# Kernel optimization log

Measured on AMD Instinct MI355X. Metric: run time of the kernel, lower is better.

## Reference

```python
import jax, jax.numpy as jnp
import numpy as np

B, C, H, W = 4, 8, 64, 64
C8 = C // 8  # = 1, required for the residual broadcast in PAM


def _conv1x1(x, w, b):
    # x: [B,C,H,W], w: [O,C], b: [O] -> [B,O,H,W]
    return jnp.einsum('bchw,oc->bohw', x, w) + b[None, :, None, None]


def setup_inputs() -> dict:
    key = jax.random.key(0)
    ks = jax.random.split(key, 13)
    s_c = 1.0 / np.sqrt(C)
    inp = {'x': jax.random.normal(ks[0], (B, C, H, W), jnp.float32)}
    # CAM: three 1x1 convs C->C
    inp['cam_wq'] = jax.random.normal(ks[1], (C, C), jnp.float32) * s_c
    inp['cam_bq'] = jnp.zeros((C,), jnp.float32)
    inp['cam_wk'] = jax.random.normal(ks[2], (C, C), jnp.float32) * s_c
    inp['cam_bk'] = jnp.zeros((C,), jnp.float32)
    inp['cam_wv'] = jax.random.normal(ks[3], (C, C), jnp.float32) * s_c
    inp['cam_bv'] = jnp.zeros((C,), jnp.float32)
    # PAM: three 1x1 convs C->C//8
    inp['pam_wq'] = jax.random.normal(ks[4], (C8, C), jnp.float32) * s_c
    inp['pam_bq'] = jnp.zeros((C8,), jnp.float32)
    inp['pam_wk'] = jax.random.normal(ks[5], (C8, C), jnp.float32) * s_c
    inp['pam_bk'] = jnp.zeros((C8,), jnp.float32)
    inp['pam_wv'] = jax.random.normal(ks[6], (C8, C), jnp.float32) * s_c
    inp['pam_bv'] = jnp.zeros((C8,), jnp.float32)
    return inp


def reference(x, cam_wq, cam_bq, cam_wk, cam_bk, cam_wv, cam_bv,
              pam_wq, pam_bq, pam_wk, pam_bk, pam_wv, pam_bv):
    b, c, h, w = x.shape
    hw = h * w

    # ---- Channel Attention Module (C x C attention) ----
    q = _conv1x1(x, cam_wq, cam_bq).reshape(b, c, hw)            # [B,C,HW]
    k = _conv1x1(x, cam_wk, cam_bk).reshape(b, c, hw)            # [B,C,HW]
    v = _conv1x1(x, cam_wv, cam_bv).reshape(b, c, hw)            # [B,C,HW]
    attn_c = jax.nn.softmax(jnp.einsum('bcn,bdn->bcd', q, k), axis=-1)  # [B,C,C]
    out_cam = jnp.einsum('bcd,bdn->bcn', attn_c, v).reshape(b, c, h, w) + x

    # ---- Pixel Attention Module (HW x HW attention, C//8 channels) ----
    pq = _conv1x1(x, pam_wq, pam_bq).reshape(b, -1, hw)          # [B,C8,HW]
    pk = _conv1x1(x, pam_wk, pam_bk).reshape(b, -1, hw)          # [B,C8,HW]
    pv = _conv1x1(x, pam_wv, pam_bv).reshape(b, -1, hw)          # [B,C8,HW]
    attn_p = jax.nn.softmax(jnp.einsum('bcn,bcm->bnm', pq, pk), axis=-1)  # [B,HW,HW]
    # out = v @ attn^T  -> [B,C8,HW]; residual broadcasts C8=1 against C
    out_p = jnp.einsum('bcm,bnm->bcn', pv, attn_p).reshape(b, c // 8, h, w)
    out_pam = out_p + x                                          # broadcast [B,1,H,W]+[B,C,H,W]

    return out_pam + out_cam
```

## Files before the change

### kernel.cpp

```cpp
#include <hip/hip_runtime.h>

#define CC 8
#define HW 4096
#define L2E 1.4426950408889634f

typedef __attribute__((ext_vector_type(4))) float f32x4;

__global__ __launch_bounds__(64) void kGram(const float* __restrict__ x,
                                            float* __restrict__ ws)
{
  const int b = blockIdx.x >> 6, chunk = blockIdx.x & 63;
  const int ln = threadIdx.x;
  const int n = chunk * 64 + ln;
  const float* xb = x + b * CC * HW;

  float xv[CC];
  #pragma unroll
  for (int c = 0; c < CC; ++c) xv[c] = xb[c * HW + n];

  float acc[44];
  {
    int k = 0;
    #pragma unroll
    for (int c = 0; c < CC; ++c) {
      #pragma unroll
      for (int d = c; d < CC; ++d) { acc[k] = xv[c] * xv[d]; ++k; }
    }
    #pragma unroll
    for (int c = 0; c < CC; ++c) acc[36 + c] = xv[c];
  }
  #pragma unroll
  for (int i = 0; i < 44; ++i) {
    float v = acc[i];
    #pragma unroll
    for (int off = 32; off > 0; off >>= 1) v += __shfl_xor(v, off, 64);
    acc[i] = v;
  }
  if (ln == 0) {
    #pragma unroll
    for (int i = 0; i < 44; ++i) ws[blockIdx.x * 44 + i] = acc[i];
  }
}

__global__ __launch_bounds__(512) void kMain(
    const float* __restrict__ x,
    const float* __restrict__ cwq, const float* __restrict__ cbq,
    const float* __restrict__ cwk, const float* __restrict__ cbk,
    const float* __restrict__ cwv, const float* __restrict__ cbv,
    const float* __restrict__ pwq, const float* __restrict__ pbq,
    const float* __restrict__ pwk, const float* __restrict__ pbk,
    const float* __restrict__ pwv, const float* __restrict__ pbv,
    const float* __restrict__ ws, float* __restrict__ out)
{
  const int b = blockIdx.x >> 6, tile = blockIdx.x & 63;
  const int n0 = tile * 64;
  const int t = threadIdx.x, ln = t & 63;
  const int wid = __builtin_amdgcn_readfirstlane(t >> 6);

  __shared__ __align__(16) float kv[HW * 2];
  __shared__ float redd[8][64], redn[8][64];
  __shared__ float gpart[8][44];
  __shared__ float sums[44], Gl[64], Ll[64], Al[64], Mp[64], cvs[8], outp[64];

  const float* xb = x + b * CC * HW;

  {
    const int m8 = t * 8;
    f32x4 xa[CC], xc[CC];
    #pragma unroll
    for (int c = 0; c < CC; ++c) {
      xa[c] = *(const f32x4*)(xb + c * HW + m8);
      xc[c] = *(const f32x4*)(xb + c * HW + m8 + 4);
    }
    f32x4 o0, o1, o2, o3;
    #pragma unroll
    for (int j = 0; j < 8; ++j) {
      float kk = pbk[0], vv = pbv[0];
      #pragma unroll
      for (int c = 0; c < CC; ++c) {
        const float xv = (j < 4) ? xa[c][j & 3] : xc[c][j & 3];
        kk = fmaf(pwk[c], xv, kk);
        vv = fmaf(pwv[c], xv, vv);
      }
      kk *= L2E;
      if (j == 0) { o0[0] = kk; o0[1] = vv; }
      else if (j == 1) { o0[2] = kk; o0[3] = vv; }
      else if (j == 2) { o1[0] = kk; o1[1] = vv; }
      else if (j == 3) { o1[2] = kk; o1[3] = vv; }
      else if (j == 4) { o2[0] = kk; o2[1] = vv; }
      else if (j == 5) { o2[2] = kk; o2[3] = vv; }
      else if (j == 6) { o3[0] = kk; o3[1] = vv; }
      else             { o3[2] = kk; o3[3] = vv; }
    }
    f32x4* kv4 = (f32x4*)kv;
    kv4[t * 4 + 0] = o0; kv4[t * 4 + 1] = o1;
    kv4[t * 4 + 2] = o2; kv4[t * 4 + 3] = o3;
  }

  float xn[CC];
  #pragma unroll
  for (int c = 0; c < CC; ++c) xn[c] = xb[c * HW + n0 + ln];
  float a = pbq[0];
  #pragma unroll
  for (int c = 0; c < CC; ++c) a = fmaf(pwq[c], xn[c], a);

  if (ln < 44) {
    const float* g = ws + (b * 64 + wid * 8) * 44 + ln;
    float s = 0.f;
    #pragma unroll
    for (int r = 0; r < 8; ++r) s += g[r * 44];
    gpart[wid][ln] = s;
  }
  __syncthreads();

  {
    const f32x4* kvw = ((const f32x4*)kv) + (wid << 8);
    float dA = 0, dB = 0, dC = 0, dD = 0;
    float nA = 0, nB = 0, nC = 0, nD = 0;
    #pragma unroll 2
    for (int i = 0; i < 256; i += 4) {
      const f32x4 p0 = kvw[i], p1 = kvw[i + 1], p2 = kvw[i + 2], p3 = kvw[i + 3];
      float e;
      e = __builtin_amdgcn_exp2f(a * p0[0]); dA += e; nA = fmaf(e, p0[1], nA);
      e = __builtin_amdgcn_exp2f(a * p0[2]); dA += e; nA = fmaf(e, p0[3], nA);
      e = __builtin_amdgcn_exp2f(a * p1[0]); dB += e; nB = fmaf(e, p1[1], nB);
      e = __builtin_amdgcn_exp2f(a * p1[2]); dB += e; nB = fmaf(e, p1[3], nB);
      e = __builtin_amdgcn_exp2f(a * p2[0]); dC += e; nC = fmaf(e, p2[1], nC);
      e = __builtin_amdgcn_exp2f(a * p2[2]); dC += e; nC = fmaf(e, p2[3], nC);
      e = __builtin_amdgcn_exp2f(a * p3[0]); dD += e; nD = fmaf(e, p3[1], nD);
      e = __builtin_amdgcn_exp2f(a * p3[2]); dD += e; nD = fmaf(e, p3[3], nD);
    }
    redd[wid][ln] = (dA + dB) + (dC + dD);
    redn[wid][ln] = (nA + nB) + (nC + nD);
  }
  __syncthreads();

  if (t < 64) {
    float D = 0.f, N = 0.f;
    #pragma unroll
    for (int s = 0; s < 8; ++s) { D += redd[s][t]; N += redn[s][t]; }
    outp[t] = N / D;
  }
  if (t < 44) {
    float s = 0.f;
    #pragma unroll
    for (int w = 0; w < 8; ++w) s += gpart[w][t];
    sums[t] = s;
  }
  __syncthreads();

  const int c = ln >> 3, d = ln & 7;
  if (t < 64) {
    const int lo = min(c, d), hi = max(c, d);
    Gl[t] = sums[lo * 8 + hi - lo * (lo + 1) / 2];
  }
  __syncthreads();

  float Lv = 0.f;
  if (t < 64) {
    float qs = 0.f, ks = 0.f;
    #pragma unroll
    for (int e = 0; e < 8; ++e) {
      qs = fmaf(cwq[c * 8 + e], sums[36 + e], qs);
      ks = fmaf(cwk[d * 8 + e], sums[36 + e], ks);
    }
    float A = 0.f;
    #pragma unroll
    for (int e = 0; e < 8; ++e) {
      float inner = 0.f;
      #pragma unroll
      for (int f = 0; f < 8; ++f) inner = fmaf(Gl[e * 8 + f], cwk[d * 8 + f], inner);
      A = fmaf(cwq[c * 8 + e], inner, A);
    }
    Lv = A + qs * cbk[d] + cbq[c] * ks + 4096.f * cbq[c] * cbk[d];
    Ll[t] = Lv;
  }
  __syncthreads();

  if (t < 64) {
    float mx = -INFINITY;
    #pragma unroll
    for (int f = 0; f < 8; ++f) mx = fmaxf(mx, Ll[c * 8 + f]);
    float ssum = 0.f;
    #pragma unroll
    for (int f = 0; f < 8; ++f) ssum += __expf(Ll[c * 8 + f] - mx);
    Al[t] = __expf(Lv - mx) / ssum;
  }
  __syncthreads();

  if (t < 64) {
    float M = 0.f;
    #pragma unroll
    for (int f = 0; f < 8; ++f) M = fmaf(Al[c * 8 + f], cwv[f * 8 + d], M);
    if (d == c) M += 2.f;
    Mp[t] = M;
    if (d == 0) {
      float cvv = 0.f;
      #pragma unroll
      for (int f = 0; f < 8; ++f) cvv = fmaf(Al[c * 8 + f], cbv[f], cvv);
      cvs[c] = cvv;
    }
  }
  __syncthreads();

  {
    float o = cvs[wid] + outp[ln];
    #pragma unroll
    for (int dd = 0; dd < 8; ++dd) o = fmaf(Mp[wid * 8 + dd], xn[dd], o);
    out[(b * 8 + wid) * HW + n0 + ln] = o;
  }
}

extern "C" void kernel_launch(void* const* d_in, const int* in_sizes, int n_in,
                              void* d_out, int out_size, void* d_ws, size_t ws_size,
                              hipStream_t stream) {
  const float* x   = (const float*)d_in[0];
  const float* cwq = (const float*)d_in[1];
  const float* cbq = (const float*)d_in[2];
  const float* cwk = (const float*)d_in[3];
  const float* cbk = (const float*)d_in[4];
  const float* cwv = (const float*)d_in[5];
  const float* cbv = (const float*)d_in[6];
  const float* pwq = (const float*)d_in[7];
  const float* pbq = (const float*)d_in[8];
  const float* pwk = (const float*)d_in[9];
  const float* pbk = (const float*)d_in[10];
  const float* pwv = (const float*)d_in[11];
  const float* pbv = (const float*)d_in[12];
  float* ws  = (float*)d_ws;
  float* out = (float*)d_out;

  hipLaunchKernelGGL(kGram, dim3(256), dim3(64), 0, stream, x, ws);
  hipLaunchKernelGGL(kMain, dim3(256), dim3(512), 0, stream,
                     x, cwq, cbq, cwk, cbk, cwv, cbv,
                     pwq, pbq, pwk, pbk, pwv, pbv, ws, out);
}
```

Baseline: 24.24 us.

## Fuse Gram-statistics kernel into main kernel with redundant per-block DPP reduction

Removes the separate Gram kernel and its workspace round trip. Each block of the main kernel now computes the channel Gram matrix and channel sums for its whole batch from the x values it already loads, reducing them within each wave using DPP row operations and then across waves in shared memory. This trades one kernel launch and the global-memory dependency for redundant per-block arithmetic and higher register pressure from keeping the loaded x vectors live.

```diff
diff --git a/kernel.cpp b/kernel.cpp
--- a/kernel.cpp
+++ b/kernel.cpp
@@ -6,43 +6,21 @@
 
 typedef __attribute__((ext_vector_type(4))) float f32x4;
 
-__global__ __launch_bounds__(64) void kGram(const float* __restrict__ x,
-                                            float* __restrict__ ws)
-{
-  const int b = blockIdx.x >> 6, chunk = blockIdx.x & 63;
-  const int ln = threadIdx.x;
-  const int n = chunk * 64 + ln;
-  const float* xb = x + b * CC * HW;
-
-  float xv[CC];
-  #pragma unroll
-  for (int c = 0; c < CC; ++c) xv[c] = xb[c * HW + n];
-
-  float acc[44];
-  {
-    int k = 0;
-    #pragma unroll
-    for (int c = 0; c < CC; ++c) {
-      #pragma unroll
-      for (int d = c; d < CC; ++d) { acc[k] = xv[c] * xv[d]; ++k; }
-    }
-    #pragma unroll
-    for (int c = 0; c < CC; ++c) acc[36 + c] = xv[c];
-  }
-  #pragma unroll
-  for (int i = 0; i < 44; ++i) {
-    float v = acc[i];
-    #pragma unroll
-    for (int off = 32; off > 0; off >>= 1) v += __shfl_xor(v, off, 64);
-    acc[i] = v;
-  }
-  if (ln == 0) {
-    #pragma unroll
-    for (int i = 0; i < 44; ++i) ws[blockIdx.x * 44 + i] = acc[i];
-  }
+static __device__ __forceinline__ float dpp_sum64(float v) {
+#define DPPSTEP(CTRL, RM, BM)                                              \
+  v += __int_as_float(__builtin_amdgcn_update_dpp(                         \
+      0, __float_as_int(v), CTRL, RM, BM, true));
+  DPPSTEP(0x111, 0xf, 0xf)
+  DPPSTEP(0x112, 0xf, 0xf)
+  DPPSTEP(0x114, 0xf, 0xe)
+  DPPSTEP(0x118, 0xf, 0xc)
+  DPPSTEP(0x142, 0xa, 0xf)
+  DPPSTEP(0x143, 0xc, 0xf)
+#undef DPPSTEP
+  return v;
 }
 
-__global__ __launch_bounds__(512) void kMain(
+__global__ __launch_bounds__(512) void kFused(
     const float* __restrict__ x,
     const float* __restrict__ cwq, const float* __restrict__ cbq,
     const float* __restrict__ cwk, const float* __restrict__ cbk,
@@ -50,7 +28,7 @@
     const float* __restrict__ pwq, const float* __restrict__ pbq,
     const float* __restrict__ pwk, const float* __restrict__ pbk,
     const float* __restrict__ pwv, const float* __restrict__ pbv,
-    const float* __restrict__ ws, float* __restrict__ out)
+    float* __restrict__ out)
 {
   const int b = blockIdx.x >> 6, tile = blockIdx.x & 63;
   const int n0 = tile * 64;
@@ -64,9 +42,9 @@
 
   const float* xb = x + b * CC * HW;
 
+  f32x4 xa[CC], xc[CC];
   {
     const int m8 = t * 8;
-    f32x4 xa[CC], xc[CC];
     #pragma unroll
     for (int c = 0; c < CC; ++c) {
       xa[c] = *(const f32x4*)(xb + c * HW + m8);
@@ -97,6 +75,32 @@
     kv4[t * 4 + 2] = o2; kv4[t * 4 + 3] = o3;
   }
 
+  {
+    float acc[44];
+    #pragma unroll
+    for (int i = 0; i < 44; ++i) acc[i] = 0.f;
+    #pragma unroll
+    for (int j = 0; j < 8; ++j) {
+      float xv[CC];
+      #pragma unroll
+      for (int c = 0; c < CC; ++c) xv[c] = (j < 4) ? xa[c][j & 3] : xc[c][j & 3];
+      int k = 0;
+      #pragma unroll
+      for (int c = 0; c < CC; ++c) {
+        #pragma unroll
+        for (int d = c; d < CC; ++d) { acc[k] = fmaf(xv[c], xv[d], acc[k]); ++k; }
+      }
+      #pragma unroll
+      for (int c = 0; c < CC; ++c) acc[36 + c] += xv[c];
+    }
+    #pragma unroll
+    for (int i = 0; i < 44; ++i) acc[i] = dpp_sum64(acc[i]);
+    if (ln == 63) {
+      #pragma unroll
+      for (int i = 0; i < 44; ++i) gpart[wid][i] = acc[i];
+    }
+  }
+
   float xn[CC];
   #pragma unroll
   for (int c = 0; c < CC; ++c) xn[c] = xb[c * HW + n0 + ln];
@@ -104,13 +108,6 @@
   #pragma unroll
   for (int c = 0; c < CC; ++c) a = fmaf(pwq[c], xn[c], a);
 
-  if (ln < 44) {
-    const float* g = ws + (b * 64 + wid * 8) * 44 + ln;
-    float s = 0.f;
-    #pragma unroll
-    for (int r = 0; r < 8; ++r) s += g[r * 44];
-    gpart[wid][ln] = s;
-  }
   __syncthreads();
 
   {
@@ -227,11 +224,9 @@
   const float* pbk = (const float*)d_in[10];
   const float* pwv = (const float*)d_in[11];
   const float* pbv = (const float*)d_in[12];
-  float* ws  = (float*)d_ws;
   float* out = (float*)d_out;
 
-  hipLaunchKernelGGL(kGram, dim3(256), dim3(64), 0, stream, x, ws);
-  hipLaunchKernelGGL(kMain, dim3(256), dim3(512), 0, stream,
+  hipLaunchKernelGGL(kFused, dim3(256), dim3(512), 0, stream,
                      x, cwq, cbq, cwk, cbk, cwv, cbv,
-                     pwq, pbq, pwk, pbk, pwv, pbv, ws, out);
+                     pwq, pbq, pwk, pbk, pwv, pbv, out);
 }
```

After: 21.63 us. 1.12x faster.
